# Optimization experiments

Measured on AMD Instinct MI355X. Metric: run time of the kernel, lower is better.

## Reference

```python
import jax, jax.numpy as jnp
import numpy as np
from jax import lax

B, C, H, W = 64, 384, 28, 28
E, K, R = 3, 2, 8          # num_experts, top_k, lora rank
HID = 4 * C                # ConvNeXt MLP hidden
EPS = 1e-6
SCALING = 8.0 / 8.0        # alpha / r


def setup_inputs() -> dict:
    key = jax.random.key(0)
    ks = jax.random.split(key, 18)
    N = B * H * W
    f32 = jnp.float32
    inp = {
        "x": jax.random.normal(ks[0], (B, C, H, W), f32),
        "conv_w": jax.random.normal(ks[1], (C, 1, 7, 7), f32) * 0.05,
        "conv_b": jax.random.normal(ks[2], (C,), f32) * 0.02,
        "norm_g": 1.0 + jax.random.normal(ks[3], (C,), f32) * 0.02,
        "norm_b": jax.random.normal(ks[4], (C,), f32) * 0.02,
        "dom_g": jax.random.normal(ks[5], (E, C), f32) * 0.02,
        "dom_b": jax.random.normal(ks[6], (E, C), f32) * 0.02,
        "fc1_w": jax.random.normal(ks[7], (C, HID), f32) * (C ** -0.5),
        "fc1_b": jax.random.normal(ks[8], (HID,), f32) * 0.02,
        "fc2_w": jax.random.normal(ks[9], (HID, C), f32) * (HID ** -0.5),
        "fc2_b": jax.random.normal(ks[10], (C,), f32) * 0.02,
        "w_down": jax.random.normal(ks[11], (E, C, R), f32) * (C ** -0.5),
        "w_up": jax.random.normal(ks[12], (E, R, C), f32) * 0.02,
        "gamma": jax.random.normal(ks[13], (C,), f32) * 0.1,
        "routing_weights": jax.nn.softmax(jax.random.normal(ks[14], (B, E), f32), axis=-1),
        "topk_probs": jax.nn.softmax(jax.random.normal(ks[15], (N, K), f32), axis=-1),
        "topk_indices": jax.random.randint(ks[16], (N, K), 0, E),
    }
    return inp


def _forward(x, conv_w, conv_b, norm_g, norm_b, dom_g, dom_b,
             fc1_w, fc1_b, fc2_w, fc2_b, w_down, w_up, gamma,
             routing_weights, topk_probs, topk_indices):
    shortcut = x
    # depthwise 7x7 conv, NCHW, SAME padding
    y = lax.conv_general_dilated(
        x, conv_w, window_strides=(1, 1), padding=((3, 3), (3, 3)),
        feature_group_count=C,
        dimension_numbers=("NCHW", "OIHW", "NCHW"))
    y = y + conv_b[None, :, None, None]
    y = jnp.transpose(y, (0, 2, 3, 1))  # [B, H, W, C] channels-last path

    # ParallelMoELayerNorm: orig LN + sum_i w_i * LN_i(x). All LNs share eps,
    # so normalize once and fuse affine params per-sample.
    mu = jnp.mean(y, axis=-1, keepdims=True)
    var = jnp.mean(jnp.square(y - mu), axis=-1, keepdims=True)
    xhat = (y - mu) * lax.rsqrt(var + EPS)
    g_eff = norm_g[None, :] + routing_weights @ dom_g   # [B, C]
    b_eff = norm_b[None, :] + routing_weights @ dom_b   # [B, C]
    y = xhat * g_eff[:, None, None, :] + b_eff[:, None, None, :]

    # base ConvNeXt MLP (exact GELU, as torch nn.GELU)
    h = jax.nn.gelu(jnp.einsum("bhwc,cf->bhwf", y, fc1_w) + fc1_b,
                    approximate=False)
    orig_out = jnp.einsum("bhwf,fc->bhwc", h, fc2_w) + fc2_b

    # MoE LoRA: dense per-expert rank-8 compute, combined with top-k weights.
    # Equivalent math to the gather/matmul/scatter-add loop in the source.
    y_flat = y.reshape(-1, C)                                   # [N, C]
    down = jnp.einsum("nc,ecr->enr", y_flat, w_down)            # [E, N, R]
    up = jnp.einsum("enr,erc->enc", jax.nn.gelu(down, approximate=False), w_up)
    # combine weights: comb[n, e] = sum_k topk_probs[n, k] * (topk_indices[n,k]==e)
    comb = jnp.sum(jax.nn.one_hot(topk_indices, E, dtype=y.dtype)
                   * topk_probs[..., None], axis=1)             # [N, E]
    moe_out = jnp.einsum("enc,ne->nc", up * SCALING, comb)
    y = orig_out + moe_out.reshape(B, H, W, C)

    y = jnp.transpose(y, (0, 3, 1, 2))  # back to NCHW
    y = gamma[None, :, None, None] * y  # layer scale; drop_path = identity (eval)
    return y + shortcut


def reference(x, conv_w, conv_b, norm_g, norm_b, dom_g, dom_b,
              fc1_w, fc1_b, fc2_w, fc2_b, w_down, w_up, gamma,
              routing_weights, topk_probs, topk_indices):
    return _forward(x, conv_w, conv_b, norm_g, norm_b, dom_g, dom_b,
                    fc1_w, fc1_b, fc2_w, fc2_b, w_down, w_up, gamma,
                    routing_weights, topk_probs, topk_indices)
```

## Files before the change

kernel.cpp:

```cpp
#include <hip/hip_runtime.h>
#include <hip/hip_bf16.h>
#include <cstdint>
#include <cstddef>

constexpr int cB   = 64;
constexpr int cC   = 384;
constexpr int cH   = 28;
constexpr int cW   = 28;
constexpr int cHID = 1536;
constexpr int cNTOK = cB * cH * cW;
constexpr int cKP   = cHID + 32;
constexpr int cCH   = 2;
constexpr int cMR   = cNTOK / cCH;

typedef __attribute__((ext_vector_type(8))) short bf16x8;
typedef __attribute__((ext_vector_type(4))) float f32x4;

__device__ __forceinline__ float gelu_f(float x) {
  float u = 1.5957691216057308f * x * (1.0f + 0.044715f * x * x);
  float e = __expf(-u);
  return x / (1.0f + e);
}

__device__ __forceinline__ float bf16_to_f(unsigned short s) {
  return __uint_as_float(((unsigned)s) << 16);
}
__device__ __forceinline__ unsigned short f_to_bf16(float v) {
  __hip_bfloat16 hb = __float2bfloat16(v);
  return *reinterpret_cast<unsigned short*>(&hb);
}

__device__ __forceinline__ void gload_lds16(const void* g, void* l) {
  __builtin_amdgcn_global_load_lds(
      (const __attribute__((address_space(1))) unsigned int*)g,
      (__attribute__((address_space(3))) unsigned int*)l, 16, 0, 0);
}

__device__ __forceinline__ int xcd_remap(int b, int nwg) {
  int qn = nwg >> 3, rm = nwg & 7;
  int xcd = b & 7, off = b >> 3;
  return (xcd < rm) ? xcd * (qn + 1) + off
                    : rm * (qn + 1) + (xcd - rm) * qn + off;
}

__global__ __launch_bounds__(256) void prep_eff(
    const float* __restrict__ ng, const float* __restrict__ nb,
    const float* __restrict__ dg, const float* __restrict__ db,
    const float* __restrict__ rw, float* __restrict__ geff, float* __restrict__ beff) {
  int i = blockIdx.x * 256 + threadIdx.x;
  if (i >= cB * cC) return;
  int b = i / cC, c = i - b * cC;
  float g = ng[c], bb = nb[c];
#pragma unroll
  for (int e = 0; e < 3; ++e) {
    float r = rw[b * 3 + e];
    g += r * dg[e * cC + c];
    bb += r * db[e * cC + c];
  }
  geff[i] = g;
  beff[i] = bb;
}

__global__ __launch_bounds__(256) void transpose_bf16(
    const float* __restrict__ w, __hip_bfloat16* __restrict__ wt, int R0, int C0) {
  __shared__ float t[64][65];
  int c0 = blockIdx.x * 64, r0 = blockIdx.y * 64;
  for (int i = threadIdx.x; i < 64 * 64; i += 256) {
    int r = i >> 6, c = i & 63;
    t[r][c] = w[(size_t)(r0 + r) * C0 + c0 + c];
  }
  __syncthreads();
  for (int i = threadIdx.x; i < 64 * 64; i += 256) {
    int c = i >> 6, r = i & 63;
    wt[(size_t)(c0 + c) * R0 + r0 + r] = __float2bfloat16(t[r][c]);
  }
}

__global__ __launch_bounds__(256) void build_fc2t(
    const float* __restrict__ fc2w, const float* __restrict__ wu,
    __hip_bfloat16* __restrict__ fc2t) {
  int i = blockIdx.x * 256 + threadIdx.x;
  if (i >= cC * cKP) return;
  int c = i / cKP, k = i - c * cKP;
  float v = 0.f;
  if (k < cHID) v = fc2w[(size_t)k * cC + c];
  else {
    int j = k - cHID;
    if (j < 24) v = wu[(size_t)(j >> 3) * 8 * cC + (size_t)(j & 7) * cC + c];
  }
  fc2t[i] = __float2bfloat16(v);
}

__global__ __launch_bounds__(256) void build_wdt(
    const float* __restrict__ wd, __hip_bfloat16* __restrict__ wdt) {
  int i = blockIdx.x * 256 + threadIdx.x;
  if (i >= 32 * cC) return;
  int j = i / cC, c = i - j * cC;
  float v = 0.f;
  if (j < 24) v = wd[(size_t)(j >> 3) * cC * 8 + (size_t)c * 8 + (j & 7)];
  wdt[i] = __float2bfloat16(v);
}

constexpr int cPL = 4;
__global__ __launch_bounds__(128) void conv_dw(
    const float* __restrict__ x, const float* __restrict__ cw,
    const float* __restrict__ cb, __hip_bfloat16* __restrict__ out) {
  int pb = blockIdx.x * cPL;
  int c0 = pb % cC;
  __shared__ __align__(16) float tile[cPL][34][38];
  __shared__ float wsm[cPL][49];
  const int tid = threadIdx.x;

  float2 z2 = {0.f, 0.f};
  for (int i = tid; i < cPL * 34 * 38 / 2; i += 128)
    ((float2*)tile)[i] = z2;
  __syncthreads();

  for (int i = tid; i < cPL * 196; i += 128) {
    int p = i / 196, q = i - p * 196;
    int r = q / 7, cl = (q - r * 7) * 4;
    float4 v = *(const float4*)&x[(size_t)(pb + p) * 784 + r * 28 + cl];
    float* dst = &tile[p][r + 3][cl + 4];
    *(float2*)dst = make_float2(v.x, v.y);
    *(float2*)(dst + 2) = make_float2(v.z, v.w);
  }
  for (int i = tid; i < cPL * 49; i += 128) {
    int p = i / 49, k = i - p * 49;
    wsm[p][k] = cw[(size_t)(c0 + p) * 49 + k];
  }
  __syncthreads();

  if (tid < cPL * 28) {
    int p = tid / 28, r = tid - p * 28;
    float acc[28];
    float cbv = cb[c0 + p];
#pragma unroll
    for (int w = 0; w < 28; ++w) acc[w] = cbv;
    for (int dh = 0; dh < 7; ++dh) {
      float rowv[36];
      const float* rp = &tile[p][r + dh][0];
#pragma unroll
      for (int k = 0; k < 18; ++k)
        ((float2*)rowv)[k] = *(const float2*)(rp + k * 2);
      float w7[7];
#pragma unroll
      for (int dw = 0; dw < 7; ++dw) w7[dw] = wsm[p][dh * 7 + dw];
#pragma unroll
      for (int w = 0; w < 28; ++w)
#pragma unroll
        for (int dw = 0; dw < 7; ++dw)
          acc[w] += rowv[w + dw + 1] * w7[dw];
    }
    unsigned short* op = (unsigned short*)out + (size_t)(pb + p) * 784 + r * 28;
#pragma unroll
    for (int k = 0; k < 7; ++k) {
      ushort4 s;
      s.x = f_to_bf16(acc[k * 4 + 0]);
      s.y = f_to_bf16(acc[k * 4 + 1]);
      s.z = f_to_bf16(acc[k * 4 + 2]);
      s.w = f_to_bf16(acc[k * 4 + 3]);
      *(ushort4*)&op[k * 4] = s;
    }
  }
}

__global__ __launch_bounds__(256) void ln_affine(
    const __hip_bfloat16* __restrict__ convout, const float* __restrict__ geff,
    const float* __restrict__ beff, __hip_bfloat16* __restrict__ y) {
  int bh = blockIdx.x;
  int b = bh / cH;
  int hrow = bh - b * cH;
  __shared__ float t[cC * 29];
  const unsigned short* src =
      (const unsigned short*)convout + (size_t)b * cC * (cH * cW) + (size_t)hrow * cW;
  for (int i = threadIdx.x; i < cC * 7; i += 256) {
    int c = i / 7, wq = (i - c * 7) * 4;
    ushort4 v = *(const ushort4*)&src[(size_t)c * (cH * cW) + wq];
    t[c * 29 + wq + 0] = bf16_to_f(v.x);
    t[c * 29 + wq + 1] = bf16_to_f(v.y);
    t[c * 29 + wq + 2] = bf16_to_f(v.z);
    t[c * 29 + wq + 3] = bf16_to_f(v.w);
  }
  __syncthreads();
  int wave = threadIdx.x >> 6, lane = threadIdx.x & 63;
  const float* gp = geff + (size_t)b * cC;
  const float* bp = beff + (size_t)b * cC;
  for (int w = wave; w < cW; w += 4) {
    float v[6], s = 0.f, s2 = 0.f;
#pragma unroll
    for (int j = 0; j < 6; ++j) {
      v[j] = t[(lane + 64 * j) * 29 + w];
      s += v[j];
      s2 += v[j] * v[j];
    }
#pragma unroll
    for (int d = 32; d; d >>= 1) {
      s += __shfl_xor(s, d);
      s2 += __shfl_xor(s2, d);
    }
    float mu = s * (1.0f / cC);
    float var = s2 * (1.0f / cC) - mu * mu;
    float rstd = rsqrtf(var + 1e-6f);
    size_t n = (size_t)bh * cW + w;
#pragma unroll
    for (int j = 0; j < 6; ++j) {
      int c = lane + 64 * j;
      float val = (v[j] - mu) * rstd * gp[c] + bp[c];
      y[n * cC + c] = __float2bfloat16(val);
    }
  }
}

template <int DO_GELU>
__global__ __launch_bounds__(256) void gemm_bt(
    const __hip_bfloat16* __restrict__ A, int lda,
    const __hip_bfloat16* __restrict__ Bt,
    const float* __restrict__ bias,
    __hip_bfloat16* __restrict__ Cb, int ldc,
    int M, int N, int K, int NT_N) {
  __shared__ __align__(16) __hip_bfloat16 As[3][128 * 32];
  __shared__ __align__(16) __hip_bfloat16 Bs[3][128 * 32];

  const int bid = xcd_remap(blockIdx.x, gridDim.x);
  const int gsz = 8 * NT_N;
  const int g = bid / gsz;
  const int q = bid - g * gsz;
  const int mi = g * 8 + q / NT_N;
  const int ni = q - (q / NT_N) * NT_N;
  const int m0 = mi * 128, n0 = ni * 128;

  const int tid = threadIdx.x;
  const int lane = tid & 63;
  const int wid = tid >> 6;
  const int wm = wid >> 1, wn = wid & 1;

  const int base0 = wid * 2048;
  const int base1 = base0 + 1024;
  const int off0 = base0 + lane * 16, off1 = base1 + lane * 16;
  const int row0 = off0 >> 6, col0 = (off0 >> 1) & 31;
  const int row1 = off1 >> 6, col1 = (off1 >> 1) & 31;
  const __hip_bfloat16* pa0 = &A[(size_t)(m0 + row0) * lda + col0];
  const __hip_bfloat16* pa1 = &A[(size_t)(m0 + row1) * lda + col1];
  const __hip_bfloat16* pb0 = &Bt[(size_t)(n0 + row0) * K + col0];
  const __hip_bfloat16* pb1 = &Bt[(size_t)(n0 + row1) * K + col1];

  const int nt = K >> 5;

#define STAGE(BUF)                                        \
  do {                                                    \
    gload_lds16(pa0, (char*)As[BUF] + base0);             \
    gload_lds16(pa1, (char*)As[BUF] + base1);             \
    gload_lds16(pb0, (char*)Bs[BUF] + base0);             \
    gload_lds16(pb1, (char*)Bs[BUF] + base1);             \
    pa0 += 32; pa1 += 32; pb0 += 32; pb1 += 32;           \
  } while (0)

  STAGE(0);
  STAGE(1);
  asm volatile("s_waitcnt vmcnt(4)" ::: "memory");
  __builtin_amdgcn_sched_barrier(0);
  __builtin_amdgcn_s_barrier();
  __builtin_amdgcn_sched_barrier(0);

  f32x4 acc[4][4] = {};
  int cur = 0, nxt2 = 2;
  for (int t = 0; t < nt; ++t) {
    if (t + 2 < nt) STAGE(nxt2);

    bf16x8 af[4], bfr[4];
#pragma unroll
    for (int i = 0; i < 4; ++i)
      af[i] = *(const bf16x8*)&As[cur][(wm * 64 + i * 16 + (lane & 15)) * 32 + (lane >> 4) * 8];
#pragma unroll
    for (int i = 0; i < 4; ++i)
      bfr[i] = *(const bf16x8*)&Bs[cur][(wn * 64 + i * 16 + (lane & 15)) * 32 + (lane >> 4) * 8];
#pragma unroll
    for (int i = 0; i < 4; ++i)
#pragma unroll
      for (int j = 0; j < 4; ++j)
        acc[i][j] = __builtin_amdgcn_mfma_f32_16x16x32_bf16(af[i], bfr[j], acc[i][j], 0, 0, 0);

    if (t + 2 < nt) {
      asm volatile("s_waitcnt vmcnt(4)" ::: "memory");
    } else if (t + 1 < nt) {
      asm volatile("s_waitcnt vmcnt(0)" ::: "memory");
    }
    if (t + 1 < nt) {
      __builtin_amdgcn_sched_barrier(0);
      __builtin_amdgcn_s_barrier();
      __builtin_amdgcn_sched_barrier(0);
    }
    cur = (cur == 2) ? 0 : cur + 1;
    nxt2 = (nxt2 == 2) ? 0 : nxt2 + 1;
  }
#undef STAGE

#pragma unroll
  for (int i = 0; i < 4; ++i) {
    int row = m0 + wm * 64 + i * 16 + (lane >> 4) * 4;
#pragma unroll
    for (int j = 0; j < 4; ++j) {
      int col = n0 + wn * 64 + j * 16 + (lane & 15);
      float bv = bias[col];
#pragma unroll
      for (int r = 0; r < 4; ++r) {
        float vv = acc[i][j][r] + bv;
        if (DO_GELU) vv = gelu_f(vv);
        Cb[(size_t)(row + r) * ldc + col] = __float2bfloat16(vv);
      }
    }
  }
}

__global__ __launch_bounds__(256) void lora_down(
    const __hip_bfloat16* __restrict__ y,
    const __hip_bfloat16* __restrict__ wdt,
    const float* __restrict__ probs,
    const int* __restrict__ inds,
    __hip_bfloat16* __restrict__ h) {
  __shared__ __align__(16) __hip_bfloat16 As[2][128 * 32];
  __shared__ __align__(16) __hip_bfloat16 Bsm[32 * 384];
  const int tid = threadIdx.x, lane = tid & 63, wid = tid >> 6;
  const int n0 = blockIdx.x * 128;

  for (int i = tid; i < 32 * 384 / 8; i += 256)
    ((bf16x8*)Bsm)[i] = ((const bf16x8*)wdt)[i];

  const int base0 = wid * 2048, base1 = base0 + 1024;
  const int off0 = base0 + lane * 16, off1 = base1 + lane * 16;
  const int row0 = off0 >> 6, col0 = (off0 >> 1) & 31;
  const int row1 = off1 >> 6, col1 = (off1 >> 1) & 31;
  const __hip_bfloat16* pa0 = &y[(size_t)(n0 + row0) * cC + col0];
  const __hip_bfloat16* pa1 = &y[(size_t)(n0 + row1) * cC + col1];

  const int nt = cC >> 5;
  gload_lds16(pa0, (char*)As[0] + base0);
  gload_lds16(pa1, (char*)As[0] + base1);
  pa0 += 32; pa1 += 32;
  __syncthreads();

  f32x4 acc[2][2] = {};
  int cur = 0;
  for (int t = 0; t < nt; ++t, cur ^= 1) {
    if (t + 1 < nt) {
      gload_lds16(pa0, (char*)As[cur ^ 1] + base0);
      gload_lds16(pa1, (char*)As[cur ^ 1] + base1);
      pa0 += 32; pa1 += 32;
    }
    int kt = t * 32;
    bf16x8 af[2], bfr[2];
#pragma unroll
    for (int i = 0; i < 2; ++i)
      af[i] = *(const bf16x8*)&As[cur][(wid * 32 + i * 16 + (lane & 15)) * 32 + (lane >> 4) * 8];
#pragma unroll
    for (int j = 0; j < 2; ++j)
      bfr[j] = *(const bf16x8*)&Bsm[(j * 16 + (lane & 15)) * 384 + kt + (lane >> 4) * 8];
#pragma unroll
    for (int i = 0; i < 2; ++i)
#pragma unroll
      for (int j = 0; j < 2; ++j)
        acc[i][j] = __builtin_amdgcn_mfma_f32_16x16x32_bf16(af[i], bfr[j], acc[i][j], 0, 0, 0);
    __syncthreads();
  }

#pragma unroll
  for (int i = 0; i < 2; ++i) {
#pragma unroll
    for (int j = 0; j < 2; ++j) {
      int colb = j * 16 + (lane & 15);
#pragma unroll
      for (int r = 0; r < 4; ++r) {
        int n = n0 + wid * 32 + i * 16 + (lane >> 4) * 4 + r;
        float zv = 0.f;
        if (colb < 24) {
          int e = colb >> 3;
          float comb = 0.f;
          if (inds[(size_t)n * 2] == e)     comb += probs[(size_t)n * 2];
          if (inds[(size_t)n * 2 + 1] == e) comb += probs[(size_t)n * 2 + 1];
          zv = comb * gelu_f(acc[i][j][r]);
        }
        h[(size_t)n * cKP + cHID + colb] = __float2bfloat16(zv);
      }
    }
  }
}

__global__ __launch_bounds__(256) void final_out(
    const __hip_bfloat16* __restrict__ tmp, const float* __restrict__ x,
    const float* __restrict__ gamma, float* __restrict__ out) {
  int bh = blockIdx.x;
  int b = bh / cH, hrow = bh - b * cH;
  __shared__ float t[cW * 385];
  const __hip_bfloat16* src = tmp + (size_t)bh * cW * cC;
  for (int i = threadIdx.x; i < cW * cC / 8; i += 256) {
    bf16x8 v = ((const bf16x8*)src)[i];
    int base = i * 8;
    int w = base / cC, c = base - w * cC;
#pragma unroll
    for (int k = 0; k < 8; ++k)
      t[w * 385 + c + k] = bf16_to_f((unsigned short)v[k]);
  }
  __syncthreads();
  const float* xb = x + (size_t)b * cC * (cH * cW) + (size_t)hrow * cW;
  float* ob = out + (size_t)b * cC * (cH * cW) + (size_t)hrow * cW;
  for (int i = threadIdx.x; i < cC * cW; i += 256) {
    int c = i / cW, w = i - c * cW;
    ob[(size_t)c * (cH * cW) + w] = gamma[c] * t[w * 385 + c] + xb[(size_t)c * (cH * cW) + w];
  }
}

extern "C" void kernel_launch(void* const* d_in, const int* in_sizes, int n_in,
                              void* d_out, int out_size, void* d_ws, size_t ws_size,
                              hipStream_t stream) {
  const float* x      = (const float*)d_in[0];
  const float* conv_w = (const float*)d_in[1];
  const float* conv_b = (const float*)d_in[2];
  const float* norm_g = (const float*)d_in[3];
  const float* norm_b = (const float*)d_in[4];
  const float* dom_g  = (const float*)d_in[5];
  const float* dom_b  = (const float*)d_in[6];
  const float* fc1_w  = (const float*)d_in[7];
  const float* fc1_b  = (const float*)d_in[8];
  const float* fc2_w  = (const float*)d_in[9];
  const float* fc2_b  = (const float*)d_in[10];
  const float* w_down = (const float*)d_in[11];
  const float* w_up   = (const float*)d_in[12];
  const float* gamma  = (const float*)d_in[13];
  const float* rw     = (const float*)d_in[14];
  const float* tkp    = (const float*)d_in[15];
  const int*   tki    = (const int*)d_in[16];
  float* out = (float*)d_out;

  char* ws = (char*)d_ws;
  __hip_bfloat16* y      = (__hip_bfloat16*)(ws + 0);
  __hip_bfloat16* tmpb   = (__hip_bfloat16*)(ws + 38535168);
  char*           hslot  = ws + 77070336;
  __hip_bfloat16* h      = (__hip_bfloat16*)hslot;
  __hip_bfloat16* convb  = (__hip_bfloat16*)hslot;
  __hip_bfloat16* fc1t   = (__hip_bfloat16*)(ws + 155746304);
  __hip_bfloat16* fc2t   = (__hip_bfloat16*)(ws + 156925952);
  __hip_bfloat16* wdt    = (__hip_bfloat16*)(ws + 158130176);
  float*          geff   = (float*)(ws + 158154752);
  float*          beff   = (float*)(ws + 158253056);

  prep_eff<<<(cB * cC + 255) / 256, 256, 0, stream>>>(norm_g, norm_b, dom_g, dom_b, rw, geff, beff);
  transpose_bf16<<<dim3(cHID / 64, cC / 64), 256, 0, stream>>>(fc1_w, fc1t, cC, cHID);
  build_fc2t<<<(cC * cKP + 255) / 256, 256, 0, stream>>>(fc2_w, w_up, fc2t);
  build_wdt<<<(32 * cC + 255) / 256, 256, 0, stream>>>(w_down, wdt);
  conv_dw<<<cB * cC / cPL, 128, 0, stream>>>(x, conv_w, conv_b, convb);
  ln_affine<<<cB * cH, 256, 0, stream>>>(convb, geff, beff, y);

  const int NTM = cMR / 128;
  for (int ch = 0; ch < cCH; ++ch) {
    const __hip_bfloat16* ych = y + (size_t)ch * cMR * cC;
    gemm_bt<1><<<NTM * (cHID / 128), 256, 0, stream>>>(
        ych, cC, fc1t, fc1_b, h, cKP, cMR, cHID, cC, cHID / 128);
    lora_down<<<NTM, 256, 0, stream>>>(
        ych, wdt, tkp + (size_t)ch * cMR * 2, tki + (size_t)ch * cMR * 2, h);
    gemm_bt<0><<<NTM * (cC / 128), 256, 0, stream>>>(
        h, cKP, fc2t, fc2_b, tmpb + (size_t)ch * cMR * cC, cC, cMR, cC, cKP, cC / 128);
  }

  final_out<<<cB * cH, 256, 0, stream>>>(tmpb, x, gamma, out);
}
```

Measured before the change: 417.3 us.

## Enlarge GEMM tiles to 256x128 with 8 waves, K-step 64 and swizzled LDS

Replaces the 128x128, 4-wave, K=32 GEMM with a 256x128 tile, 512 threads and 64-wide K stages. LDS uses an XOR swizzle to avoid bank conflicts, and A/B staging is split across the two K halves with raised priority around MFMA blocks. The LoRA padding of the hidden dimension grows to 64 so K divides the new step, and the extra columns are zero-filled. The larger LDS footprint limits occupancy, and the padded K adds some wasted work.

After: 429.9 us. +3.0%, slower.

```diff
diff --git a/kernel.cpp b/kernel.cpp
--- a/kernel.cpp
+++ b/kernel.cpp
@@ -9,7 +9,7 @@
 constexpr int cW   = 28;
 constexpr int cHID = 1536;
 constexpr int cNTOK = cB * cH * cW;
-constexpr int cKP   = cHID + 32;
+constexpr int cKP   = cHID + 64;
 constexpr int cCH   = 2;
 constexpr int cMR   = cNTOK / cCH;
 
@@ -212,14 +212,14 @@
 }
 
 template <int DO_GELU>
-__global__ __launch_bounds__(256) void gemm_bt(
+__global__ __launch_bounds__(512) void gemm8(
     const __hip_bfloat16* __restrict__ A, int lda,
     const __hip_bfloat16* __restrict__ Bt,
     const float* __restrict__ bias,
     __hip_bfloat16* __restrict__ Cb, int ldc,
     int M, int N, int K, int NT_N) {
-  __shared__ __align__(16) __hip_bfloat16 As[3][128 * 32];
-  __shared__ __align__(16) __hip_bfloat16 Bs[3][128 * 32];
+  __shared__ __align__(16) __hip_bfloat16 As[3][256 * 64];
+  __shared__ __align__(16) __hip_bfloat16 Bs[3][128 * 64];
 
   const int bid = xcd_remap(blockIdx.x, gridDim.x);
   const int gsz = 8 * NT_N;
@@ -227,61 +227,106 @@
   const int q = bid - g * gsz;
   const int mi = g * 8 + q / NT_N;
   const int ni = q - (q / NT_N) * NT_N;
-  const int m0 = mi * 128, n0 = ni * 128;
+  const int m0 = mi * 256, n0 = ni * 128;
 
   const int tid = threadIdx.x;
   const int lane = tid & 63;
   const int wid = tid >> 6;
-  const int wm = wid >> 1, wn = wid & 1;
-
-  const int base0 = wid * 2048;
-  const int base1 = base0 + 1024;
-  const int off0 = base0 + lane * 16, off1 = base1 + lane * 16;
-  const int row0 = off0 >> 6, col0 = (off0 >> 1) & 31;
-  const int row1 = off1 >> 6, col1 = (off1 >> 1) & 31;
-  const __hip_bfloat16* pa0 = &A[(size_t)(m0 + row0) * lda + col0];
-  const __hip_bfloat16* pa1 = &A[(size_t)(m0 + row1) * lda + col1];
-  const __hip_bfloat16* pb0 = &Bt[(size_t)(n0 + row0) * K + col0];
-  const __hip_bfloat16* pb1 = &Bt[(size_t)(n0 + row1) * K + col1];
-
-  const int nt = K >> 5;
-
-#define STAGE(BUF)                                        \
-  do {                                                    \
-    gload_lds16(pa0, (char*)As[BUF] + base0);             \
-    gload_lds16(pa1, (char*)As[BUF] + base1);             \
-    gload_lds16(pb0, (char*)Bs[BUF] + base0);             \
-    gload_lds16(pb1, (char*)Bs[BUF] + base1);             \
-    pa0 += 32; pa1 += 32; pb0 += 32; pb1 += 32;           \
+  const int wm = wid >> 1;
+  const int wn = wid & 1;
+  const int l15 = lane & 15, l7 = lane & 7, lq = lane >> 4;
+
+  const __hip_bfloat16* srcA[4];
+  const __hip_bfloat16* srcB[2];
+  int dstA[4], dstB[2];
+#pragma unroll
+  for (int a = 0; a < 4; ++a) {
+    int gu = a * 512 + tid;
+    int row = gu >> 3, pu = gu & 7;
+    int u = pu ^ (row & 7);
+    srcA[a] = &A[(size_t)(m0 + row) * lda + u * 8];
+    dstA[a] = gu * 16;
+  }
+#pragma unroll
+  for (int b = 0; b < 2; ++b) {
+    int gu = b * 512 + tid;
+    int row = gu >> 3, pu = gu & 7;
+    int u = pu ^ (row & 7);
+    srcB[b] = &Bt[(size_t)(n0 + row) * K + u * 8];
+    dstB[b] = gu * 16;
+  }
+
+#define STAGE_A(BUF)                                         \
+  do {                                                       \
+    _Pragma("unroll") for (int a = 0; a < 4; ++a) {          \
+      gload_lds16(srcA[a], (char*)As[BUF] + dstA[a]);        \
+      srcA[a] += 64;                                         \
+    }                                                        \
   } while (0)
-
-  STAGE(0);
-  STAGE(1);
-  asm volatile("s_waitcnt vmcnt(4)" ::: "memory");
+#define STAGE_B(BUF)                                         \
+  do {                                                       \
+    _Pragma("unroll") for (int b = 0; b < 2; ++b) {          \
+      gload_lds16(srcB[b], (char*)Bs[BUF] + dstB[b]);        \
+      srcB[b] += 64;                                         \
+    }                                                        \
+  } while (0)
+
+  int roA[2][4], roB[2][4];
+#pragma unroll
+  for (int kh = 0; kh < 2; ++kh) {
+    int pu = (kh * 4 + lq) ^ l7;
+#pragma unroll
+    for (int i = 0; i < 4; ++i) {
+      roA[kh][i] = (wm * 64 + i * 16 + l15) * 128 + pu * 16;
+      roB[kh][i] = (wn * 64 + i * 16 + l15) * 128 + pu * 16;
+    }
+  }
+
+  const int nt = K >> 6;
+
+  STAGE_A(0); STAGE_B(0);
+  STAGE_A(1); STAGE_B(1);
+  asm volatile("s_waitcnt vmcnt(6)" ::: "memory");
   __builtin_amdgcn_sched_barrier(0);
   __builtin_amdgcn_s_barrier();
   __builtin_amdgcn_sched_barrier(0);
 
   f32x4 acc[4][4] = {};
-  int cur = 0, nxt2 = 2;
+  int cur = 0, nx2 = 2;
   for (int t = 0; t < nt; ++t) {
-    if (t + 2 < nt) STAGE(nxt2);
-
-    bf16x8 af[4], bfr[4];
+    const char* asc = (const char*)As[cur];
+    const char* bsc = (const char*)Bs[cur];
+
+    bf16x8 a0[4], b0[4];
+#pragma unroll
+    for (int i = 0; i < 4; ++i) a0[i] = *(const bf16x8*)(asc + roA[0][i]);
+#pragma unroll
+    for (int j = 0; j < 4; ++j) b0[j] = *(const bf16x8*)(bsc + roB[0][j]);
+    if (t + 2 < nt) STAGE_A(nx2);
+    __builtin_amdgcn_s_setprio(1);
 #pragma unroll
     for (int i = 0; i < 4; ++i)
-      af[i] = *(const bf16x8*)&As[cur][(wm * 64 + i * 16 + (lane & 15)) * 32 + (lane >> 4) * 8];
+#pragma unroll
+      for (int j = 0; j < 4; ++j)
+        acc[i][j] = __builtin_amdgcn_mfma_f32_16x16x32_bf16(a0[i], b0[j], acc[i][j], 0, 0, 0);
+    __builtin_amdgcn_s_setprio(0);
+
+    bf16x8 a1[4], b1[4];
+#pragma unroll
+    for (int i = 0; i < 4; ++i) a1[i] = *(const bf16x8*)(asc + roA[1][i]);
+#pragma unroll
+    for (int j = 0; j < 4; ++j) b1[j] = *(const bf16x8*)(bsc + roB[1][j]);
+    if (t + 2 < nt) STAGE_B(nx2);
+    __builtin_amdgcn_s_setprio(1);
 #pragma unroll
     for (int i = 0; i < 4; ++i)
-      bfr[i] = *(const bf16x8*)&Bs[cur][(wn * 64 + i * 16 + (lane & 15)) * 32 + (lane >> 4) * 8];
-#pragma unroll
-    for (int i = 0; i < 4; ++i)
 #pragma unroll
       for (int j = 0; j < 4; ++j)
-        acc[i][j] = __builtin_amdgcn_mfma_f32_16x16x32_bf16(af[i], bfr[j], acc[i][j], 0, 0, 0);
+        acc[i][j] = __builtin_amdgcn_mfma_f32_16x16x32_bf16(a1[i], b1[j], acc[i][j], 0, 0, 0);
+    __builtin_amdgcn_s_setprio(0);
 
     if (t + 2 < nt) {
-      asm volatile("s_waitcnt vmcnt(4)" ::: "memory");
+      asm volatile("s_waitcnt vmcnt(6)" ::: "memory");
     } else if (t + 1 < nt) {
       asm volatile("s_waitcnt vmcnt(0)" ::: "memory");
     }
@@ -291,9 +336,10 @@
       __builtin_amdgcn_sched_barrier(0);
     }
     cur = (cur == 2) ? 0 : cur + 1;
-    nxt2 = (nxt2 == 2) ? 0 : nxt2 + 1;
-  }
-#undef STAGE
+    nx2 = (nx2 == 2) ? 0 : nx2 + 1;
+  }
+#undef STAGE_A
+#undef STAGE_B
 
 #pragma unroll
   for (int i = 0; i < 4; ++i) {
@@ -380,6 +426,7 @@
           zv = comb * gelu_f(acc[i][j][r]);
         }
         h[(size_t)n * cKP + cHID + colb] = __float2bfloat16(zv);
+        h[(size_t)n * cKP + cHID + 32 + colb] = __float2bfloat16(0.f);
       }
     }
   }
@@ -437,11 +484,11 @@
   char*           hslot  = ws + 77070336;
   __hip_bfloat16* h      = (__hip_bfloat16*)hslot;
   __hip_bfloat16* convb  = (__hip_bfloat16*)hslot;
-  __hip_bfloat16* fc1t   = (__hip_bfloat16*)(ws + 155746304);
-  __hip_bfloat16* fc2t   = (__hip_bfloat16*)(ws + 156925952);
-  __hip_bfloat16* wdt    = (__hip_bfloat16*)(ws + 158130176);
-  float*          geff   = (float*)(ws + 158154752);
-  float*          beff   = (float*)(ws + 158253056);
+  __hip_bfloat16* fc1t   = (__hip_bfloat16*)(ws + 157351936);
+  __hip_bfloat16* fc2t   = (__hip_bfloat16*)(ws + 158531584);
+  __hip_bfloat16* wdt    = (__hip_bfloat16*)(ws + 159760384);
+  float*          geff   = (float*)(ws + 159784960);
+  float*          beff   = (float*)(ws + 159883264);
 
   prep_eff<<<(cB * cC + 255) / 256, 256, 0, stream>>>(norm_g, norm_b, dom_g, dom_b, rw, geff, beff);
   transpose_bf16<<<dim3(cHID / 64, cC / 64), 256, 0, stream>>>(fc1_w, fc1t, cC, cHID);
@@ -450,14 +497,14 @@
   conv_dw<<<cB * cC / cPL, 128, 0, stream>>>(x, conv_w, conv_b, convb);
   ln_affine<<<cB * cH, 256, 0, stream>>>(convb, geff, beff, y);
 
-  const int NTM = cMR / 128;
+  const int NTM8 = cMR / 256;
   for (int ch = 0; ch < cCH; ++ch) {
     const __hip_bfloat16* ych = y + (size_t)ch * cMR * cC;
-    gemm_bt<1><<<NTM * (cHID / 128), 256, 0, stream>>>(
+    gemm8<1><<<NTM8 * (cHID / 128), 512, 0, stream>>>(
         ych, cC, fc1t, fc1_b, h, cKP, cMR, cHID, cC, cHID / 128);
-    lora_down<<<NTM, 256, 0, stream>>>(
+    lora_down<<<cMR / 128, 256, 0, stream>>>(
         ych, wdt, tkp + (size_t)ch * cMR * 2, tki + (size_t)ch * cMR * 2, h);
-    gemm_bt<0><<<NTM * (cC / 128), 256, 0, stream>>>(
+    gemm8<0><<<NTM8 * (cC / 128), 512, 0, stream>>>(
         h, cKP, fc2t, fc2_b, tmpb + (size_t)ch * cMR * cC, cC, cMR, cC, cKP, cC / 128);
   }
 
```
